# Performance work log

Hardware: AMD Instinct MI355X
Metric: run time of the kernel (lower is better)

Reference implementation:

```python
import jax, jax.numpy as jnp
import numpy as np

B, T, TA = 16, 512, 1024
D_REG, D_AUD, HID, HEADS = 512, 512, 256, 4
NREG = 4  # mouth, left_eye, right_eye, nose (dict order)
N = NREG * B * T + B * TA  # total graph nodes


def _build_edges():
    # Faithful, vectorized version of build_graph's edge construction (phoneme_times=None).
    bs = np.arange(B)[:, None]
    ts = np.arange(T)[None, :]
    src, dst = [], []
    # cross-region same-timestep edges, all ordered pairs i != j (edge_attr 0)
    for i in range(NREG):
        for j in range(NREG):
            if i != j:
                n1 = i * B * T + bs * T + ts
                n2 = j * B * T + bs * T + ts
                src.append(n1.ravel()); dst.append(n2.ravel())
    # temporal edges within each region (edge_attr 1)
    tt = np.arange(T - 1)[None, :]
    for i in range(NREG):
        n1 = i * B * T + bs * T + tt
        src.append(n1.ravel()); dst.append((n1 + 1).ravel())
    # eye (region idx 1,2) -> audio alignment edges (edge_attr 3)
    t_aud = (np.arange(T)[None, :] * TA) // T
    audio_start = NREG * B * T
    for i in (1, 2):
        n_eye = i * B * T + bs * T + ts
        n_aud = audio_start + bs * TA + t_aud
        src.append(n_eye.ravel()); dst.append(np.broadcast_to(n_aud, (B, T)).ravel())
    # self loops (PyG GATConv default add_self_loops=True)
    loops = np.arange(N)
    src.append(loops); dst.append(loops)
    return np.concatenate(src).astype(np.int32), np.concatenate(dst).astype(np.int32)


def setup_inputs() -> dict:
    key = jax.random.key(0)
    ks = iter(jax.random.split(key, 48))
    def rn(shape, scale=1.0):
        return jax.random.normal(next(ks), shape, dtype=jnp.float32) * jnp.float32(scale)
    src_np, dst_np = _build_edges()
    inp = {
        'mouth': rn((B, T, D_REG)), 'left_eye': rn((B, T, D_REG)),
        'right_eye': rn((B, T, D_REG)), 'nose': rn((B, T, D_REG)),
        'audio_embeddings': rn((B, TA, D_AUD)),
    }
    s = 1.0 / np.sqrt(D_REG)
    for name in ['mouth', 'left_eye', 'right_eye', 'nose']:
        inp['w_' + name] = rn((D_REG, HID), s)
        inp['b_' + name] = jnp.zeros((HID,), jnp.float32)
    inp['w_audio'] = rn((D_AUD, HID), 1.0 / np.sqrt(D_AUD))
    inp['b_audio'] = jnp.zeros((HID,), jnp.float32)
    # GAT layers: layer 0 in=HID, layers 1,2 in=HID*HEADS; layers 0,1 concat, layer 2 averages heads
    dims_in = [HID, HID * HEADS, HID * HEADS]
    for l, din in enumerate(dims_in):
        concat = l < 2
        inp[f'W{l}'] = rn((din, HEADS * HID), 1.0 / np.sqrt(din))
        inp[f'as{l}'] = rn((HEADS, HID), 0.1)
        inp[f'ad{l}'] = rn((HEADS, HID), 0.1)
        inp[f'bias{l}'] = jnp.zeros((HEADS * HID,) if concat else (HID,), jnp.float32)
    inp['ln_g'] = jnp.ones((HID,), jnp.float32)
    inp['ln_b'] = jnp.zeros((HID,), jnp.float32)
    inp['src'] = jnp.asarray(src_np)
    inp['dst'] = jnp.asarray(dst_np)
    return inp


def _gat(x, W, a_s, a_d, bias, src, dst, concat):
    # PyG GATConv (eval mode): gather -> per-head attention softmax over dst -> scatter-add
    H, C = a_s.shape
    h = (x @ W).reshape(-1, H, C)                      # [N,H,C]
    alpha_s = jnp.sum(h * a_s, -1)                     # [N,H]
    alpha_d = jnp.sum(h * a_d, -1)                     # [N,H]
    e = jax.nn.leaky_relu(alpha_s[src] + alpha_d[dst], 0.2)  # [E,H]
    m = jax.ops.segment_max(e, dst, num_segments=N)
    ex = jnp.exp(e - m[dst])
    denom = jax.ops.segment_sum(ex, dst, num_segments=N)
    alpha = ex / (denom[dst] + jnp.float32(1e-16))
    out = jax.ops.segment_sum(h[src] * alpha[:, :, None], dst, num_segments=N)  # [N,H,C]
    out = out.reshape(-1, H * C) if concat else out.mean(1)
    return out + bias


def _forward(mouth, left_eye, right_eye, nose, audio_embeddings,
             w_mouth, b_mouth, w_left_eye, b_left_eye, w_right_eye, b_right_eye,
             w_nose, b_nose, w_audio, b_audio,
             W0, as0, ad0, bias0, W1, as1, ad1, bias1, W2, as2, ad2, bias2,
             ln_g, ln_b, src, dst):
    x = jnp.concatenate([
        (mouth @ w_mouth + b_mouth).reshape(B * T, HID),
        (left_eye @ w_left_eye + b_left_eye).reshape(B * T, HID),
        (right_eye @ w_right_eye + b_right_eye).reshape(B * T, HID),
        (nose @ w_nose + b_nose).reshape(B * T, HID),
        (audio_embeddings @ w_audio + b_audio).reshape(B * TA, HID),
    ], axis=0)                                          # [N,HID]
    x = _gat(x, W0, as0, ad0, bias0, src, dst, True)    # [N,HID*HEADS]
    x = _gat(x, W1, as1, ad1, bias1, src, dst, True)    # [N,HID*HEADS]
    x = _gat(x, W2, as2, ad2, bias2, src, dst, False)   # [N,HID]
    mu = x.mean(-1, keepdims=True)
    var = jnp.mean(jnp.square(x - mu), -1, keepdims=True)
    x = (x - mu) / jnp.sqrt(var + jnp.float32(1e-5)) * ln_g + ln_b
    nodes_pb = NREG * T + TA
    return x.reshape(B, nodes_pb, HID).mean(1)          # [B,HID]


def reference(mouth, left_eye, right_eye, nose, audio_embeddings,
              w_mouth, b_mouth, w_left_eye, b_left_eye, w_right_eye, b_right_eye,
              w_nose, b_nose, w_audio, b_audio,
              W0, as0, ad0, bias0, W1, as1, ad1, bias1, W2, as2, ad2, bias2,
              ln_g, ln_b, src, dst):
    return _forward(mouth, left_eye, right_eye, nose, audio_embeddings,
                    w_mouth, b_mouth, w_left_eye, b_left_eye, w_right_eye, b_right_eye,
                    w_nose, b_nose, w_audio, b_audio,
                    W0, as0, ad0, bias0, W1, as1, ad1, bias1, W2, as2, ad2, bias2,
                    ln_g, ln_b, src, dst)
```

## Files before the change

### kernel.cpp

```cpp
#include <hip/hip_runtime.h>


typedef unsigned short u16;
typedef unsigned int u32;
typedef __bf16 bf16x8 __attribute__((ext_vector_type(8)));
typedef float f32x4 __attribute__((ext_vector_type(4)));

#define ASYNC16(gp, lp)                                                        \
  __builtin_amdgcn_global_load_lds(                                            \
      (const __attribute__((address_space(1))) void*)(gp),                     \
      (__attribute__((address_space(3))) void*)(lp), 16, 0, 0)

__device__ __forceinline__ u16 f2bf(float f) {
  union { float f; u32 u; } v; v.f = f;
  u32 u = v.u + 0x7FFFu + ((v.u >> 16) & 1u);
  return (u16)(u >> 16);
}
__device__ __forceinline__ float bf2f(u16 x) {
  union { u32 u; float f; } v; v.u = ((u32)x) << 16;
  return v.f;
}
__device__ __forceinline__ float4 cvt4(ushort4 s) {
  float4 r; r.x = bf2f(s.x); r.y = bf2f(s.y); r.z = bf2f(s.z); r.w = bf2f(s.w);
  return r;
}
__device__ __forceinline__ float lrelu(float v) { return v > 0.f ? v : 0.2f * v; }
__device__ __forceinline__ float dot4(float4 a, float4 b) {
  return a.x * b.x + a.y * b.y + a.z * b.z + a.w * b.w;
}
__device__ __forceinline__ float wred(float v) {
#pragma unroll
  for (int off = 32; off; off >>= 1) v += __shfl_down(v, off);
  return v;
}
__device__ __forceinline__ float wredx(float v) {
#pragma unroll
  for (int off = 32; off; off >>= 1) v += __shfl_xor(v, off);
  return v;
}

struct PK { const float* W[8]; u16* P[8]; int KB[8]; int NN[8]; int st[9]; };
__global__ __launch_bounds__(256) void pack_kernel(PK p) {
  const int f = blockIdx.x * 4 + (threadIdx.x >> 6);
  const int lane = threadIdx.x & 63;
  int e = 0;
  while (f >= p.st[e + 1]) ++e;
  const int local = f - p.st[e];
  const int KB = p.KB[e], N = p.NN[e];
  const int nt = local / KB, kb = local % KB;
  const float* W = p.W[e] + (size_t)(kb * 32 + (lane >> 4) * 8) * N + nt * 16 + (lane & 15);
  u16* dst = p.P[e] + ((size_t)local * 64 + lane) * 8;
  u16 o[8];
#pragma unroll
  for (int j = 0; j < 8; ++j) o[j] = f2bf(W[(size_t)j * N]);
  *(uint4*)dst = *(uint4*)o;
}

__global__ __launch_bounds__(256) void gemm_kernel(
    const u16* __restrict__ A, const u16* __restrict__ Bp, u16* __restrict__ C,
    int K, int ldc) {
  __shared__ __align__(16) u16 As[2][2][128 * 32];
  const int KB = K >> 5;
  const int KB2 = K >> 6;
  const int w = blockIdx.y * 8 + blockIdx.x;
  const int xcd = w & 7, m = w >> 3;
  const int blockCol = (m & 7) * 128;
  const int blockRow = ((m >> 3) * 8 + xcd) * 128;
  const int tid = threadIdx.x;
  const int wave = tid >> 6, lane = tid & 63;
  const int wr = (wave >> 1) * 64, wc = (wave & 1) * 64;
  const int lr = lane & 15, lq = lane >> 4;
  const int sRow = wave * 16 + (lane >> 2);
  const int sGc = (lane & 3) ^ ((sRow >> 1) & 3);
  const size_t aOff0 = (size_t)(blockRow + sRow) * K + sGc * 8;
  const size_t aOff1 = aOff0 + (size_t)64 * K;
  const int ldsOff0 = wave * 512;
  const int ldsOff1 = 2048 + wave * 512;

  const u16* Bn[4];
#pragma unroll
  for (int ni = 0; ni < 4; ++ni)
    Bn[ni] = Bp + ((size_t)(((blockCol + wc) >> 4) + ni) * KB) * 512 + lane * 8;

  f32x4 acc[4][4] = {};

#pragma unroll
  for (int h = 0; h < 2; ++h) {
    ASYNC16(A + aOff0 + h * 32, As[0][h] + ldsOff0);
    ASYNC16(A + aOff1 + h * 32, As[0][h] + ldsOff1);
  }
  __syncthreads();

  for (int kb2 = 0; kb2 < KB2; ++kb2) {
    const int cb = kb2 & 1;
    bf16x8 bfr[2][4];
#pragma unroll
    for (int h = 0; h < 2; ++h)
#pragma unroll
      for (int ni = 0; ni < 4; ++ni)
        bfr[h][ni] = *(const bf16x8*)(Bn[ni] + (size_t)(kb2 * 2 + h) * 512);
    if (kb2 + 1 < KB2) {
      const size_t k1 = (size_t)(kb2 + 1) * 64;
#pragma unroll
      for (int h = 0; h < 2; ++h) {
        ASYNC16(A + aOff0 + k1 + h * 32, As[cb ^ 1][h] + ldsOff0);
        ASYNC16(A + aOff1 + k1 + h * 32, As[cb ^ 1][h] + ldsOff1);
      }
    }
#pragma unroll
    for (int h = 0; h < 2; ++h) {
      const u16* cur = As[cb][h];
      bf16x8 af[4];
#pragma unroll
      for (int mi = 0; mi < 4; ++mi) {
        const int R = wr + mi * 16 + lr;
        const int cp = lq ^ ((R >> 1) & 3);
        af[mi] = *(const bf16x8*)(cur + R * 32 + cp * 8);
      }
#pragma unroll
      for (int mi = 0; mi < 4; ++mi)
#pragma unroll
        for (int ni = 0; ni < 4; ++ni)
          acc[mi][ni] = __builtin_amdgcn_mfma_f32_16x16x32_bf16(af[mi], bfr[h][ni],
                                                                acc[mi][ni], 0, 0, 0);
    }
    __syncthreads();
  }
#pragma unroll
  for (int mi = 0; mi < 4; ++mi)
#pragma unroll
    for (int ni = 0; ni < 4; ++ni) {
      const int col = blockCol + wc + ni * 16 + lr;
#pragma unroll
      for (int r = 0; r < 4; ++r) {
        const int row = blockRow + wr + mi * 16 + lq * 4 + r;
        C[(size_t)row * ldc + col] = f2bf(acc[mi][ni][r]);
      }
    }
}

struct ProjArgs { const float* x[5]; const u16* w[5]; const float* b[5]; };
__global__ __launch_bounds__(256) void proj_kernel(ProjArgs pa,
                                                   u16* __restrict__ C) {
  __shared__ __align__(16) u16 As[128 * 32];
  const int blockRow = blockIdx.y * 128, blockCol = blockIdx.x * 128;
  const int reg = blockRow >= 32768 ? 4 : (blockRow >> 13);
  const int regBase = reg == 4 ? 32768 : reg * 8192;
  const float* Af = pa.x[reg] + (size_t)(blockRow - regBase) * 512;
  const u16* Bp = pa.w[reg];
  const int tid = threadIdx.x;
  const int wave = tid >> 6, lane = tid & 63;
  const int wr = (wave >> 1) * 64, wc = (wave & 1) * 64;
  const int lr = lane & 15, lq = lane >> 4;
  const int rr = tid >> 2;
  const int cphys = tid & 3;
  const int sGc = cphys ^ ((tid >> 3) & 3);

  const u16* Bn[4];
#pragma unroll
  for (int ni = 0; ni < 4; ++ni)
    Bn[ni] = Bp + ((size_t)(((blockCol + wc) >> 4) + ni) * 16) * 512 + lane * 8;

  f32x4 acc[4][4] = {};

  for (int k0 = 0; k0 < 512; k0 += 32) {
    __syncthreads();
    bf16x8 bfr[4];
#pragma unroll
    for (int ni = 0; ni < 4; ++ni)
      bfr[ni] = *(const bf16x8*)(Bn[ni] + (size_t)k0 * 16);
#pragma unroll
    for (int i = 0; i < 2; ++i) {
      const int row = i * 64 + rr;
      const float* ap = Af + (size_t)row * 512 + k0 + sGc * 8;
      float4 f0 = *(const float4*)(ap);
      float4 f1 = *(const float4*)(ap + 4);
      uint4 pk;
      pk.x = (u32)f2bf(f0.x) | ((u32)f2bf(f0.y) << 16);
      pk.y = (u32)f2bf(f0.z) | ((u32)f2bf(f0.w) << 16);
      pk.z = (u32)f2bf(f1.x) | ((u32)f2bf(f1.y) << 16);
      pk.w = (u32)f2bf(f1.z) | ((u32)f2bf(f1.w) << 16);
      *(uint4*)(&As[row * 32 + cphys * 8]) = pk;
    }
    __syncthreads();
    bf16x8 af[4];
#pragma unroll
    for (int mi = 0; mi < 4; ++mi) {
      const int R = wr + mi * 16 + lr;
      const int cp = lq ^ ((R >> 1) & 3);
      af[mi] = *(const bf16x8*)(&As[R * 32 + cp * 8]);
    }
#pragma unroll
    for (int mi = 0; mi < 4; ++mi)
#pragma unroll
      for (int ni = 0; ni < 4; ++ni)
        acc[mi][ni] = __builtin_amdgcn_mfma_f32_16x16x32_bf16(af[mi], bfr[ni],
                                                              acc[mi][ni], 0, 0, 0);
  }
  const float* bias = pa.b[reg];
#pragma unroll
  for (int mi = 0; mi < 4; ++mi)
#pragma unroll
    for (int ni = 0; ni < 4; ++ni) {
      const int col = blockCol + wc + ni * 16 + lr;
      const float bv = bias[col];
#pragma unroll
      for (int r = 0; r < 4; ++r) {
        const int row = blockRow + wr + mi * 16 + lq * 4 + r;
        C[(size_t)row * 256 + col] = f2bf(acc[mi][ni][r] + bv);
      }
    }
}

template <bool MEAN>
__global__ __launch_bounds__(256) void agg_kernel(
    const u16* __restrict__ h, const float* __restrict__ a_s,
    const float* __restrict__ a_d, const float* __restrict__ bias,
    void* __restrict__ out) {
  extern __shared__ float red[];
  const int tid = threadIdx.x;
  const int head = tid >> 6, lane = tid & 63;
  const int c4 = tid * 4;
  const float4 sa = *(const float4*)(a_s + c4);
  const float4 da = *(const float4*)(a_d + c4);
  __shared__ float asL[4][4], adL[4][4], apL[4][4], aeS[4], aeD[4];
  __shared__ float alpha[4][4][5], alphaA[4][3];

  const int bt = blockIdx.x;
  const int b = bt >> 9, t = bt & 511;
  const bool hasPrev = t > 0;
  const int btp = hasPrev ? bt - 1 : bt;
  const int nodeE = 32768 + b * 1024 + 2 * t;
  const int nodeO = nodeE + 1;

  ushort4 rv[4], rp[4], raeR, raoR;
#pragma unroll
  for (int r = 0; r < 4; ++r)
    rv[r] = *(const ushort4*)(h + (size_t)(r * 8192 + bt) * 1024 + c4);
  raeR = *(const ushort4*)(h + (size_t)nodeE * 1024 + c4);
  raoR = *(const ushort4*)(h + (size_t)nodeO * 1024 + c4);
#pragma unroll
  for (int r = 0; r < 4; ++r)
    rp[r] = *(const ushort4*)(h + (size_t)(r * 8192 + btp) * 1024 + c4);

  float4 hv[4], hp[4];
#pragma unroll
  for (int r = 0; r < 4; ++r) hv[r] = cvt4(rv[r]);
  float4 hae = cvt4(raeR), hao = cvt4(raoR);
#pragma unroll
  for (int r = 0; r < 4; ++r) hp[r] = cvt4(rp[r]);

#pragma unroll
  for (int r = 0; r < 4; ++r) {
    float ss = wred(dot4(hv[r], sa));
    float dd = wred(dot4(hv[r], da));
    float sp = hasPrev ? wred(dot4(hp[r], sa)) : 0.f;
    if (lane == 0) { asL[r][head] = ss; adL[r][head] = dd; apL[r][head] = sp; }
  }
  {
    float se = wred(dot4(hae, sa));
    float de = wred(dot4(hae, da));
    if (lane == 0) { aeS[head] = se; aeD[head] = de; }
  }
  __syncthreads();
  if (tid < 16) {
    const int j = tid >> 2, hh = tid & 3;
    const float ad = adL[j][hh];
    float e[5];
#pragma unroll
    for (int r = 0; r < 4; ++r) e[r] = lrelu(asL[r][hh] + ad);
    int cnt = 4;
    if (hasPrev) { e[4] = lrelu(apL[j][hh] + ad); cnt = 5; }
    float mx = e[0];
    for (int k = 1; k < cnt; ++k) mx = fmaxf(mx, e[k]);
    float s = 0.f, ex[5];
    for (int k = 0; k < cnt; ++k) { ex[k] = __expf(e[k] - mx); s += ex[k]; }
    const float inv = 1.f / (s + 1e-16f);
#pragma unroll
    for (int k = 0; k < 5; ++k) alpha[j][hh][k] = (k < cnt) ? ex[k] * inv : 0.f;
  } else if (tid < 20) {
    const int hh = tid - 16;
    const float ad = aeD[hh];
    const float e0 = lrelu(aeS[hh] + ad);
    const float e1 = lrelu(asL[1][hh] + ad);
    const float e2 = lrelu(asL[2][hh] + ad);
    const float mx = fmaxf(e0, fmaxf(e1, e2));
    const float x0 = __expf(e0 - mx), x1 = __expf(e1 - mx), x2 = __expf(e2 - mx);
    const float inv = 1.f / (x0 + x1 + x2 + 1e-16f);
    alphaA[hh][0] = x0 * inv; alphaA[hh][1] = x1 * inv; alphaA[hh][2] = x2 * inv;
  }
  __syncthreads();

  float4 av[6];
#pragma unroll
  for (int j = 0; j < 4; ++j) {
    const float* al = &alpha[j][head][0];
    float4 acc;
    acc.x = al[0] * hv[0].x + al[1] * hv[1].x + al[2] * hv[2].x + al[3] * hv[3].x;
    acc.y = al[0] * hv[0].y + al[1] * hv[1].y + al[2] * hv[2].y + al[3] * hv[3].y;
    acc.z = al[0] * hv[0].z + al[1] * hv[1].z + al[2] * hv[2].z + al[3] * hv[3].z;
    acc.w = al[0] * hv[0].w + al[1] * hv[1].w + al[2] * hv[2].w + al[3] * hv[3].w;
    if (hasPrev) {
      const float a4 = al[4];
      acc.x += a4 * hp[j].x; acc.y += a4 * hp[j].y;
      acc.z += a4 * hp[j].z; acc.w += a4 * hp[j].w;
    }
    av[j] = acc;
  }
  {
    const float a0 = alphaA[head][0], a1 = alphaA[head][1], a2 = alphaA[head][2];
    float4 acc;
    acc.x = a0 * hae.x + a1 * hv[1].x + a2 * hv[2].x;
    acc.y = a0 * hae.y + a1 * hv[1].y + a2 * hv[2].y;
    acc.z = a0 * hae.z + a1 * hv[1].z + a2 * hv[2].z;
    acc.w = a0 * hae.w + a1 * hv[1].w + a2 * hv[2].w;
    av[4] = acc;
    av[5] = hao;
  }

  if constexpr (!MEAN) {
    const float4 bv = *(const float4*)(bias + c4);
    u16* ob = (u16*)out;
    size_t rows[6];
#pragma unroll
    for (int j = 0; j < 4; ++j) rows[j] = (size_t)(j * 8192 + bt);
    rows[4] = (size_t)nodeE; rows[5] = (size_t)nodeO;
#pragma unroll
    for (int k = 0; k < 6; ++k) {
      ushort4 o;
      o.x = f2bf(av[k].x + bv.x); o.y = f2bf(av[k].y + bv.y);
      o.z = f2bf(av[k].z + bv.z); o.w = f2bf(av[k].w + bv.w);
      *(ushort4*)(ob + rows[k] * 1024 + c4) = o;
    }
  } else {
#pragma unroll
    for (int k = 0; k < 6; ++k) *(float4*)(&red[k * 1024 + c4]) = av[k];
    __syncthreads();
    const float bb = bias[tid];
    float* of = (float*)out;
    size_t rows[6];
#pragma unroll
    for (int j = 0; j < 4; ++j) rows[j] = (size_t)(j * 8192 + bt);
    rows[4] = (size_t)nodeE; rows[5] = (size_t)nodeO;
#pragma unroll
    for (int k = 0; k < 6; ++k) {
      const float v = 0.25f * (red[k * 1024 + tid] + red[k * 1024 + tid + 256] +
                               red[k * 1024 + tid + 512] + red[k * 1024 + tid + 768]) + bb;
      of[rows[k] * 256 + tid] = v;
    }
  }
}

__global__ __launch_bounds__(256) void ln_pool_kernel(
    const float* __restrict__ xf, const float* __restrict__ g,
    const float* __restrict__ bb, float* __restrict__ part) {
  const int tid = threadIdx.x;
  const int wave = tid >> 6, lane = tid & 63;
  const int node0 = blockIdx.x * 64 + wave * 16;
  const float4 g4 = *(const float4*)(g + lane * 4);
  const float4 b4 = *(const float4*)(bb + lane * 4);
  float4 acc = {0.f, 0.f, 0.f, 0.f};
  for (int i = 0; i < 16; ++i) {
    const float4 v = *(const float4*)(xf + (size_t)(node0 + i) * 256 + lane * 4);
    const float s = wredx(v.x + v.y + v.z + v.w);
    const float q = wredx(v.x * v.x + v.y * v.y + v.z * v.z + v.w * v.w);
    const float mean = s * (1.f / 256.f);
    const float var = q * (1.f / 256.f) - mean * mean;
    const float rstd = rsqrtf(var + 1e-5f);
    acc.x += (v.x - mean) * rstd * g4.x + b4.x;
    acc.y += (v.y - mean) * rstd * g4.y + b4.y;
    acc.z += (v.z - mean) * rstd * g4.z + b4.z;
    acc.w += (v.w - mean) * rstd * g4.w + b4.w;
  }
  *(float4*)(part + (size_t)(blockIdx.x * 4 + wave) * 256 + lane * 4) = acc;
}

__global__ __launch_bounds__(256) void pool2_kernel(const float* __restrict__ part,
                                                    float* __restrict__ out) {
  const int chunk = blockIdx.x;
  const int c = threadIdx.x;
  float s = 0.f;
  for (int i = 0; i < 192; ++i) s += part[(size_t)(chunk * 192 + i) * 256 + c];
  out[chunk * 256 + c] = s * (1.f / 3072.f);
}

extern "C" void kernel_launch(void* const* d_in, const int* in_sizes, int n_in,
                              void* d_out, int out_size, void* d_ws, size_t ws_size,
                              hipStream_t stream) {
  const float* x_reg[4] = {(const float*)d_in[0], (const float*)d_in[1],
                           (const float*)d_in[2], (const float*)d_in[3]};
  const float* audio = (const float*)d_in[4];
  const float* w_reg[4] = {(const float*)d_in[5], (const float*)d_in[7],
                           (const float*)d_in[9], (const float*)d_in[11]};
  const float* b_reg[4] = {(const float*)d_in[6], (const float*)d_in[8],
                           (const float*)d_in[10], (const float*)d_in[12]};
  const float* w_aud = (const float*)d_in[13];
  const float* b_aud = (const float*)d_in[14];
  const float* Wl[3] = {(const float*)d_in[15], (const float*)d_in[19],
                        (const float*)d_in[23]};
  const float* as_in[3] = {(const float*)d_in[16], (const float*)d_in[20],
                           (const float*)d_in[24]};
  const float* ad_in[3] = {(const float*)d_in[17], (const float*)d_in[21],
                           (const float*)d_in[25]};
  const float* bias_l[3] = {(const float*)d_in[18], (const float*)d_in[22],
                            (const float*)d_in[26]};
  const float* ln_g = (const float*)d_in[27];
  const float* ln_b = (const float*)d_in[28];

  char* ws = (char*)d_ws;
  u16* h_bf = (u16*)ws;
  float* part = (float*)ws;
  u16* xb = (u16*)(ws + 100663296);
  float* xf = (float*)xb;
  u16* wt = (u16*)(ws + 201326592);

  u16* wtp[5];
  for (int r = 0; r < 5; ++r) wtp[r] = wt + (size_t)r * 131072;
  u16* wt0 = wt + 655360;
  u16* wt1 = wt + 917504;
  u16* wt2 = wt + 1966080;

  PK pk;
  for (int r = 0; r < 4; ++r) { pk.W[r] = w_reg[r]; pk.P[r] = wtp[r]; pk.KB[r] = 16; pk.NN[r] = 256; }
  pk.W[4] = w_aud; pk.P[4] = wtp[4]; pk.KB[4] = 16; pk.NN[4] = 256;
  pk.W[5] = Wl[0]; pk.P[5] = wt0; pk.KB[5] = 8;  pk.NN[5] = 1024;
  pk.W[6] = Wl[1]; pk.P[6] = wt1; pk.KB[6] = 32; pk.NN[6] = 1024;
  pk.W[7] = Wl[2]; pk.P[7] = wt2; pk.KB[7] = 32; pk.NN[7] = 1024;
  pk.st[0] = 0;
  {
    const int nfr[8] = {256, 256, 256, 256, 256, 512, 2048, 2048};
    int acc = 0;
    for (int e = 0; e < 8; ++e) { acc += nfr[e]; pk.st[e + 1] = acc; }
  }
  pack_kernel<<<pk.st[8] / 4, 256, 0, stream>>>(pk);

  ProjArgs pa;
  for (int r = 0; r < 4; ++r) { pa.x[r] = x_reg[r]; pa.w[r] = wtp[r]; pa.b[r] = b_reg[r]; }
  pa.x[4] = audio; pa.w[4] = wtp[4]; pa.b[4] = b_aud;
  proj_kernel<<<dim3(2, 384), 256, 0, stream>>>(pa, xb);

  const u16* wl[3] = {wt0, wt1, wt2};
  const int Kl[3] = {256, 1024, 1024};
  const size_t dynLds = 6 * 1024 * sizeof(float);
  for (int l = 0; l < 3; ++l) {
    gemm_kernel<<<dim3(8, 384), 256, 0, stream>>>(xb, wl[l], h_bf, Kl[l], 1024);
    if (l < 2)
      agg_kernel<false><<<8192, 256, 0, stream>>>(h_bf, as_in[l], ad_in[l],
                                                  bias_l[l], xb);
    else
      agg_kernel<true><<<8192, 256, dynLds, stream>>>(h_bf, as_in[l], ad_in[l],
                                                      bias_l[l], xf);
  }

  ln_pool_kernel<<<768, 256, 0, stream>>>(xf, ln_g, ln_b, part);
  pool2_kernel<<<16, 256, 0, stream>>>(part, (float*)d_out);
}
```

Measured before the change: 613.5 us.

## Rewrite GAT GEMM as 256x256 tile, 8-wave, 4-stage LDS pipeline

Replaces the 128x128-tile, 4-wave, double-buffered GEMM with a 256x256-tile kernel using 8 waves and a 4-deep ring of LDS buffers, where both A and B are now staged into LDS asynchronously. The K loop is split into two half-phases separated by barriers, with explicit vmcnt waits and s_setprio around the MFMA blocks so loads overlap compute. The aim is more reuse per tile and better hiding of global-memory latency. In exchange it uses 128 KB of LDS per block, limiting occupancy to one block per CU, and relies on hand-counted waitcnt values.

```diff
diff --git a/kernel.cpp b/kernel.cpp
--- a/kernel.cpp
+++ b/kernel.cpp
@@ -56,84 +56,115 @@
   *(uint4*)dst = *(uint4*)o;
 }
 
-__global__ __launch_bounds__(256) void gemm_kernel(
+__global__ __launch_bounds__(512, 1) void gemm_kernel(
     const u16* __restrict__ A, const u16* __restrict__ Bp, u16* __restrict__ C,
     int K, int ldc) {
-  __shared__ __align__(16) u16 As[2][2][128 * 32];
-  const int KB = K >> 5;
-  const int KB2 = K >> 6;
-  const int w = blockIdx.y * 8 + blockIdx.x;
-  const int xcd = w & 7, m = w >> 3;
-  const int blockCol = (m & 7) * 128;
-  const int blockRow = ((m >> 3) * 8 + xcd) * 128;
+  __shared__ __align__(16) u16 lds[4 * 16384];
+  const int NT = K >> 5;
+
+  const int orig = blockIdx.x;
+  const int x = orig & 7;
+  const int local = orig >> 3;
+  const int colTile = local & 3;
+  const int rowTile = x * 24 + (local >> 2);
+  const int blockRow = rowTile * 256;
+  const int blockCol = colTile * 256;
+
   const int tid = threadIdx.x;
   const int wave = tid >> 6, lane = tid & 63;
-  const int wr = (wave >> 1) * 64, wc = (wave & 1) * 64;
+  const int wm = wave >> 2, wn = wave & 3;
   const int lr = lane & 15, lq = lane >> 4;
-  const int sRow = wave * 16 + (lane >> 2);
-  const int sGc = (lane & 3) ^ ((sRow >> 1) & 3);
-  const size_t aOff0 = (size_t)(blockRow + sRow) * K + sGc * 8;
-  const size_t aOff1 = aOff0 + (size_t)64 * K;
-  const int ldsOff0 = wave * 512;
-  const int ldsOff1 = 2048 + wave * 512;
-
-  const u16* Bn[4];
-#pragma unroll
-  for (int ni = 0; ni < 4; ++ni)
-    Bn[ni] = Bp + ((size_t)(((blockCol + wc) >> 4) + ni) * KB) * 512 + lane * 8;
-
-  f32x4 acc[4][4] = {};
-
-#pragma unroll
-  for (int h = 0; h < 2; ++h) {
-    ASYNC16(A + aOff0 + h * 32, As[0][h] + ldsOff0);
-    ASYNC16(A + aOff1 + h * 32, As[0][h] + ldsOff1);
-  }
-  __syncthreads();
-
-  for (int kb2 = 0; kb2 < KB2; ++kb2) {
-    const int cb = kb2 & 1;
-    bf16x8 bfr[2][4];
-#pragma unroll
-    for (int h = 0; h < 2; ++h)
+  const int f0 = wave * 2, f1 = f0 + 1;
+
+  const int sR = lane >> 2;
+  const int sGc = (lane & 3) ^ ((lane >> 3) & 3);
+  const size_t aG0 = (size_t)(blockRow + f0 * 16 + sR) * K + sGc * 8;
+  const size_t aG1 = (size_t)(blockRow + f1 * 16 + sR) * K + sGc * 8;
+  const int ntBase = blockCol >> 4;
+  const size_t bG0 = (size_t)(ntBase + f0) * NT * 512 + lane * 8;
+  const size_t bG1 = (size_t)(ntBase + f1) * NT * 512 + lane * 8;
+
+  const int aFr = (wm * 128 + lr) * 32 + (lq ^ ((lr >> 1) & 3)) * 8;
+  const int bFr = wn * 2048 + lane * 8;
+
+#define STAGE_A(TS)                                                            \
+  do {                                                                         \
+    u16* db_ = &lds[((TS) & 3) * 16384];                                       \
+    ASYNC16(A + aG0 + (size_t)(TS) * 32, db_ + f0 * 512);                      \
+    ASYNC16(A + aG1 + (size_t)(TS) * 32, db_ + f1 * 512);                      \
+  } while (0)
+#define STAGE_B(TS)                                                            \
+  do {                                                                         \
+    u16* db_ = &lds[((TS) & 3) * 16384 + 8192];                                \
+    ASYNC16(Bp + bG0 + (size_t)(TS) * 512, db_ + f0 * 512);                    \
+    ASYNC16(Bp + bG1 + (size_t)(TS) * 512, db_ + f1 * 512);                    \
+  } while (0)
+
+  f32x4 acc[8][4] = {};
+
+  STAGE_A(0); STAGE_B(0);
+  STAGE_A(1); STAGE_B(1);
+  STAGE_A(2); STAGE_B(2);
+  asm volatile("s_waitcnt vmcnt(8)" ::: "memory");
+  asm volatile("s_barrier" ::: "memory");
+
+  for (int t = 0; t < NT; ++t) {
+    u16* Ab = &lds[(t & 3) * 16384];
+    u16* Bb = Ab + 8192;
+    const int ts = t + 3;
+    bf16x8 bfr[4], af[4];
+
+#pragma unroll
+    for (int ni = 0; ni < 4; ++ni)
+      bfr[ni] = *(const bf16x8*)(Bb + bFr + ni * 512);
+#pragma unroll
+    for (int i = 0; i < 4; ++i)
+      af[i] = *(const bf16x8*)(Ab + aFr + i * 512);
+    if (ts < NT) STAGE_A(ts);
+    asm volatile("s_barrier" ::: "memory");
+    __builtin_amdgcn_s_setprio(1);
+#pragma unroll
+    for (int i = 0; i < 4; ++i)
 #pragma unroll
       for (int ni = 0; ni < 4; ++ni)
-        bfr[h][ni] = *(const bf16x8*)(Bn[ni] + (size_t)(kb2 * 2 + h) * 512);
-    if (kb2 + 1 < KB2) {
-      const size_t k1 = (size_t)(kb2 + 1) * 64;
-#pragma unroll
-      for (int h = 0; h < 2; ++h) {
-        ASYNC16(A + aOff0 + k1 + h * 32, As[cb ^ 1][h] + ldsOff0);
-        ASYNC16(A + aOff1 + k1 + h * 32, As[cb ^ 1][h] + ldsOff1);
-      }
-    }
-#pragma unroll
-    for (int h = 0; h < 2; ++h) {
-      const u16* cur = As[cb][h];
-      bf16x8 af[4];
-#pragma unroll
-      for (int mi = 0; mi < 4; ++mi) {
-        const int R = wr + mi * 16 + lr;
-        const int cp = lq ^ ((R >> 1) & 3);
-        af[mi] = *(const bf16x8*)(cur + R * 32 + cp * 8);
-      }
-#pragma unroll
-      for (int mi = 0; mi < 4; ++mi)
-#pragma unroll
-        for (int ni = 0; ni < 4; ++ni)
-          acc[mi][ni] = __builtin_amdgcn_mfma_f32_16x16x32_bf16(af[mi], bfr[h][ni],
-                                                                acc[mi][ni], 0, 0, 0);
-    }
-    __syncthreads();
-  }
-#pragma unroll
-  for (int mi = 0; mi < 4; ++mi)
+        acc[i][ni] = __builtin_amdgcn_mfma_f32_16x16x32_bf16(af[i], bfr[ni],
+                                                             acc[i][ni], 0, 0, 0);
+    __builtin_amdgcn_s_setprio(0);
+    asm volatile("s_barrier" ::: "memory");
+
+#pragma unroll
+    for (int i = 0; i < 4; ++i)
+      af[i] = *(const bf16x8*)(Ab + aFr + (i + 4) * 512);
+    if (ts < NT) STAGE_B(ts);
+    if (t <= NT - 4) {
+      asm volatile("s_waitcnt vmcnt(8)" ::: "memory");
+    } else if (t == NT - 3) {
+      asm volatile("s_waitcnt vmcnt(4)" ::: "memory");
+    } else if (t == NT - 2) {
+      asm volatile("s_waitcnt vmcnt(0)" ::: "memory");
+    }
+    asm volatile("s_barrier" ::: "memory");
+    __builtin_amdgcn_s_setprio(1);
+#pragma unroll
+    for (int i = 0; i < 4; ++i)
+#pragma unroll
+      for (int ni = 0; ni < 4; ++ni)
+        acc[i + 4][ni] = __builtin_amdgcn_mfma_f32_16x16x32_bf16(af[i], bfr[ni],
+                                                                 acc[i + 4][ni], 0, 0, 0);
+    __builtin_amdgcn_s_setprio(0);
+    asm volatile("s_barrier" ::: "memory");
+  }
+#undef STAGE_A
+#undef STAGE_B
+
+#pragma unroll
+  for (int mi = 0; mi < 8; ++mi)
 #pragma unroll
     for (int ni = 0; ni < 4; ++ni) {
-      const int col = blockCol + wc + ni * 16 + lr;
+      const int col = blockCol + wn * 64 + ni * 16 + lr;
 #pragma unroll
       for (int r = 0; r < 4; ++r) {
-        const int row = blockRow + wr + mi * 16 + lq * 4 + r;
+        const int row = blockRow + wm * 128 + mi * 16 + lq * 4 + r;
         C[(size_t)row * ldc + col] = f2bf(acc[mi][ni][r]);
       }
     }
@@ -443,7 +474,7 @@
   const int Kl[3] = {256, 1024, 1024};
   const size_t dynLds = 6 * 1024 * sizeof(float);
   for (int l = 0; l < 3; ++l) {
-    gemm_kernel<<<dim3(8, 384), 256, 0, stream>>>(xb, wl[l], h_bf, Kl[l], 1024);
+    gemm_kernel<<<768, 512, 0, stream>>>(xb, wl[l], h_bf, Kl[l], 1024);
     if (l < 2)
       agg_kernel<false><<<8192, 256, 0, stream>>>(h_bf, as_in[l], ad_in[l],
                                                   bias_l[l], xb);
```

Result: no change. 618.6 us (+0.8%).

## Deepen GEMM A-tile prefetch to a 4-buffer pipeline with explicit vmcnt waits

Applied to the files above, without the earlier changes.

Replaces the double-buffered 64-wide K step in the GEMM with a four-slot ring of 32-wide A tiles in LDS, prefetching three stages ahead. It uses hand-written s_waitcnt vmcnt counts and raw s_barrier in place of __syncthreads. The aim is to hide more global-load latency and to lighten each barrier. The risk is that the hard-coded vmcnt counts must match the number of outstanding loads, B-fragment loads included, or the kernel could read LDS before the data lands.

```diff
diff --git a/kernel.cpp b/kernel.cpp
--- a/kernel.cpp
+++ b/kernel.cpp
@@ -59,9 +59,8 @@
 __global__ __launch_bounds__(256) void gemm_kernel(
     const u16* __restrict__ A, const u16* __restrict__ Bp, u16* __restrict__ C,
     int K, int ldc) {
-  __shared__ __align__(16) u16 As[2][2][128 * 32];
-  const int KB = K >> 5;
-  const int KB2 = K >> 6;
+  __shared__ __align__(16) u16 As[4][128 * 32];
+  const int NT = K >> 5;
   const int w = blockIdx.y * 8 + blockIdx.x;
   const int xcd = w & 7, m = w >> 3;
   const int blockCol = (m & 7) * 128;
@@ -80,52 +79,52 @@
   const u16* Bn[4];
 #pragma unroll
   for (int ni = 0; ni < 4; ++ni)
-    Bn[ni] = Bp + ((size_t)(((blockCol + wc) >> 4) + ni) * KB) * 512 + lane * 8;
+    Bn[ni] = Bp + ((size_t)(((blockCol + wc) >> 4) + ni) * NT) * 512 + lane * 8;
 
   f32x4 acc[4][4] = {};
 
-#pragma unroll
-  for (int h = 0; h < 2; ++h) {
-    ASYNC16(A + aOff0 + h * 32, As[0][h] + ldsOff0);
-    ASYNC16(A + aOff1 + h * 32, As[0][h] + ldsOff1);
-  }
-  __syncthreads();
-
-  for (int kb2 = 0; kb2 < KB2; ++kb2) {
-    const int cb = kb2 & 1;
-    bf16x8 bfr[2][4];
-#pragma unroll
-    for (int h = 0; h < 2; ++h)
+#define STAGE(TS)                                                              \
+  do {                                                                         \
+    u16* db_ = As[(TS) & 3];                                                   \
+    ASYNC16(A + aOff0 + (size_t)(TS) * 32, db_ + ldsOff0);                     \
+    ASYNC16(A + aOff1 + (size_t)(TS) * 32, db_ + ldsOff1);                     \
+  } while (0)
+
+  STAGE(0); STAGE(1); STAGE(2);
+  asm volatile("s_waitcnt vmcnt(4)" ::: "memory");
+  asm volatile("s_barrier" ::: "memory");
+
+  for (int t = 0; t < NT; ++t) {
+    bf16x8 bfr[4];
+#pragma unroll
+    for (int ni = 0; ni < 4; ++ni)
+      bfr[ni] = *(const bf16x8*)(Bn[ni] + (size_t)t * 512);
+    const u16* cur = As[t & 3];
+    bf16x8 af[4];
+#pragma unroll
+    for (int mi = 0; mi < 4; ++mi) {
+      const int R = wr + mi * 16 + lr;
+      const int cp = lq ^ ((R >> 1) & 3);
+      af[mi] = *(const bf16x8*)(cur + R * 32 + cp * 8);
+    }
+    if (t + 3 < NT) STAGE(t + 3);
+#pragma unroll
+    for (int mi = 0; mi < 4; ++mi)
 #pragma unroll
       for (int ni = 0; ni < 4; ++ni)
-        bfr[h][ni] = *(const bf16x8*)(Bn[ni] + (size_t)(kb2 * 2 + h) * 512);
-    if (kb2 + 1 < KB2) {
-      const size_t k1 = (size_t)(kb2 + 1) * 64;
-#pragma unroll
-      for (int h = 0; h < 2; ++h) {
-        ASYNC16(A + aOff0 + k1 + h * 32, As[cb ^ 1][h] + ldsOff0);
-        ASYNC16(A + aOff1 + k1 + h * 32, As[cb ^ 1][h] + ldsOff1);
-      }
-    }
-#pragma unroll
-    for (int h = 0; h < 2; ++h) {
-      const u16* cur = As[cb][h];
-      bf16x8 af[4];
-#pragma unroll
-      for (int mi = 0; mi < 4; ++mi) {
-        const int R = wr + mi * 16 + lr;
-        const int cp = lq ^ ((R >> 1) & 3);
-        af[mi] = *(const bf16x8*)(cur + R * 32 + cp * 8);
-      }
-#pragma unroll
-      for (int mi = 0; mi < 4; ++mi)
-#pragma unroll
-        for (int ni = 0; ni < 4; ++ni)
-          acc[mi][ni] = __builtin_amdgcn_mfma_f32_16x16x32_bf16(af[mi], bfr[h][ni],
-                                                                acc[mi][ni], 0, 0, 0);
-    }
-    __syncthreads();
-  }
+        acc[mi][ni] = __builtin_amdgcn_mfma_f32_16x16x32_bf16(af[mi], bfr[ni],
+                                                              acc[mi][ni], 0, 0, 0);
+    if (t <= NT - 4) {
+      asm volatile("s_waitcnt vmcnt(12)" ::: "memory");
+    } else if (t == NT - 3) {
+      asm volatile("s_waitcnt vmcnt(10)" ::: "memory");
+    } else if (t == NT - 2) {
+      asm volatile("s_waitcnt vmcnt(8)" ::: "memory");
+    }
+    asm volatile("s_barrier" ::: "memory");
+  }
+#undef STAGE
+
 #pragma unroll
   for (int mi = 0; mi < 4; ++mi)
 #pragma unroll
```

Result: slower. 700.4 us (+14.2%).

## Switch GAT GEMM to 32x32x16 MFMA with repacked weights; remap agg block order

Applied to the files above, without the earlier changes.

The layer GEMM now uses 32x32x16 bf16 MFMA tiles (2x2 per wave) in place of 16x16x32 (4x4 per wave), and the weight pack kernel is changed to emit fragments in the matching 32-column layout. The goal is fewer MFMA issues and fewer LDS A-fragment reads per FLOP. The aggregation kernel also permutes block indices so that neighbouring blocks are spread across XCDs, aiming at better L2 locality. The epilogue store pattern changes, and the larger accumulator tile raises register pressure.

```diff
diff --git a/kernel.cpp b/kernel.cpp
--- a/kernel.cpp
+++ b/kernel.cpp
@@ -5,6 +5,7 @@
 typedef unsigned int u32;
 typedef __bf16 bf16x8 __attribute__((ext_vector_type(8)));
 typedef float f32x4 __attribute__((ext_vector_type(4)));
+typedef float f32x16 __attribute__((ext_vector_type(16)));
 
 #define ASYNC16(gp, lp)                                                        \
   __builtin_amdgcn_global_load_lds(                                            \
@@ -48,7 +49,11 @@
   const int local = f - p.st[e];
   const int KB = p.KB[e], N = p.NN[e];
   const int nt = local / KB, kb = local % KB;
-  const float* W = p.W[e] + (size_t)(kb * 32 + (lane >> 4) * 8) * N + nt * 16 + (lane & 15);
+  const float* W;
+  if (e < 5)
+    W = p.W[e] + (size_t)(kb * 32 + (lane >> 4) * 8) * N + nt * 16 + (lane & 15);
+  else
+    W = p.W[e] + (size_t)(kb * 16 + (lane >> 5) * 8) * N + nt * 32 + (lane & 31);
   u16* dst = p.P[e] + ((size_t)local * 64 + lane) * 8;
   u16 o[8];
 #pragma unroll
@@ -60,8 +65,8 @@
     const u16* __restrict__ A, const u16* __restrict__ Bp, u16* __restrict__ C,
     int K, int ldc) {
   __shared__ __align__(16) u16 As[2][2][128 * 32];
-  const int KB = K >> 5;
   const int KB2 = K >> 6;
+  const int NT16 = K >> 4;
   const int w = blockIdx.y * 8 + blockIdx.x;
   const int xcd = w & 7, m = w >> 3;
   const int blockCol = (m & 7) * 128;
@@ -69,7 +74,7 @@
   const int tid = threadIdx.x;
   const int wave = tid >> 6, lane = tid & 63;
   const int wr = (wave >> 1) * 64, wc = (wave & 1) * 64;
-  const int lr = lane & 15, lq = lane >> 4;
+  const int lc = lane & 31, kq = lane >> 5;
   const int sRow = wave * 16 + (lane >> 2);
   const int sGc = (lane & 3) ^ ((sRow >> 1) & 3);
   const size_t aOff0 = (size_t)(blockRow + sRow) * K + sGc * 8;
@@ -77,12 +82,12 @@
   const int ldsOff0 = wave * 512;
   const int ldsOff1 = 2048 + wave * 512;
 
-  const u16* Bn[4];
-#pragma unroll
-  for (int ni = 0; ni < 4; ++ni)
-    Bn[ni] = Bp + ((size_t)(((blockCol + wc) >> 4) + ni) * KB) * 512 + lane * 8;
-
-  f32x4 acc[4][4] = {};
+  const u16* Bn[2];
+#pragma unroll
+  for (int ni = 0; ni < 2; ++ni)
+    Bn[ni] = Bp + ((size_t)(((blockCol + wc) >> 5) + ni) * NT16) * 512 + lane * 8;
+
+  f32x16 acc[2][2] = {};
 
 #pragma unroll
   for (int h = 0; h < 2; ++h) {
@@ -95,10 +100,10 @@
     const int cb = kb2 & 1;
     bf16x8 bfr[2][4];
 #pragma unroll
-    for (int h = 0; h < 2; ++h)
-#pragma unroll
-      for (int ni = 0; ni < 4; ++ni)
-        bfr[h][ni] = *(const bf16x8*)(Bn[ni] + (size_t)(kb2 * 2 + h) * 512);
+    for (int ni = 0; ni < 2; ++ni)
+#pragma unroll
+      for (int c = 0; c < 4; ++c)
+        bfr[ni][c] = *(const bf16x8*)(Bn[ni] + (size_t)(kb2 * 4 + c) * 512);
     if (kb2 + 1 < KB2) {
       const size_t k1 = (size_t)(kb2 + 1) * 64;
 #pragma unroll
@@ -110,30 +115,36 @@
 #pragma unroll
     for (int h = 0; h < 2; ++h) {
       const u16* cur = As[cb][h];
-      bf16x8 af[4];
-#pragma unroll
-      for (int mi = 0; mi < 4; ++mi) {
-        const int R = wr + mi * 16 + lr;
-        const int cp = lq ^ ((R >> 1) & 3);
-        af[mi] = *(const bf16x8*)(cur + R * 32 + cp * 8);
+      bf16x8 af[2][2];
+#pragma unroll
+      for (int mi = 0; mi < 2; ++mi) {
+        const int R = wr + mi * 32 + lc;
+        const int swz = (R >> 1) & 3;
+#pragma unroll
+        for (int kk = 0; kk < 2; ++kk) {
+          const int cp = (kk * 2 + kq) ^ swz;
+          af[mi][kk] = *(const bf16x8*)(cur + R * 32 + cp * 8);
+        }
       }
 #pragma unroll
-      for (int mi = 0; mi < 4; ++mi)
-#pragma unroll
-        for (int ni = 0; ni < 4; ++ni)
-          acc[mi][ni] = __builtin_amdgcn_mfma_f32_16x16x32_bf16(af[mi], bfr[h][ni],
-                                                                acc[mi][ni], 0, 0, 0);
+      for (int kk = 0; kk < 2; ++kk)
+#pragma unroll
+        for (int mi = 0; mi < 2; ++mi)
+#pragma unroll
+          for (int ni = 0; ni < 2; ++ni)
+            acc[mi][ni] = __builtin_amdgcn_mfma_f32_32x32x16_bf16(
+                af[mi][kk], bfr[ni][h * 2 + kk], acc[mi][ni], 0, 0, 0);
     }
     __syncthreads();
   }
 #pragma unroll
-  for (int mi = 0; mi < 4; ++mi)
-#pragma unroll
-    for (int ni = 0; ni < 4; ++ni) {
-      const int col = blockCol + wc + ni * 16 + lr;
-#pragma unroll
-      for (int r = 0; r < 4; ++r) {
-        const int row = blockRow + wr + mi * 16 + lq * 4 + r;
+  for (int mi = 0; mi < 2; ++mi)
+#pragma unroll
+    for (int ni = 0; ni < 2; ++ni) {
+      const int col = blockCol + wc + ni * 32 + lc;
+#pragma unroll
+      for (int r = 0; r < 16; ++r) {
+        const int row = blockRow + wr + mi * 32 + (r & 3) + 8 * (r >> 2) + 4 * kq;
         C[(size_t)row * ldc + col] = f2bf(acc[mi][ni][r]);
       }
     }
@@ -226,7 +237,8 @@
   __shared__ float asL[4][4], adL[4][4], apL[4][4], aeS[4], aeD[4];
   __shared__ float alpha[4][4][5], alphaA[4][3];
 
-  const int bt = blockIdx.x;
+  const int bid = blockIdx.x;
+  const int bt = ((bid & 7) << 10) | (bid >> 3);
   const int b = bt >> 9, t = bt & 511;
   const bool hasPrev = t > 0;
   const int btp = hasPrev ? bt - 1 : bt;
@@ -423,9 +435,9 @@
   PK pk;
   for (int r = 0; r < 4; ++r) { pk.W[r] = w_reg[r]; pk.P[r] = wtp[r]; pk.KB[r] = 16; pk.NN[r] = 256; }
   pk.W[4] = w_aud; pk.P[4] = wtp[4]; pk.KB[4] = 16; pk.NN[4] = 256;
-  pk.W[5] = Wl[0]; pk.P[5] = wt0; pk.KB[5] = 8;  pk.NN[5] = 1024;
-  pk.W[6] = Wl[1]; pk.P[6] = wt1; pk.KB[6] = 32; pk.NN[6] = 1024;
-  pk.W[7] = Wl[2]; pk.P[7] = wt2; pk.KB[7] = 32; pk.NN[7] = 1024;
+  pk.W[5] = Wl[0]; pk.P[5] = wt0; pk.KB[5] = 16; pk.NN[5] = 1024;
+  pk.W[6] = Wl[1]; pk.P[6] = wt1; pk.KB[6] = 64; pk.NN[6] = 1024;
+  pk.W[7] = Wl[2]; pk.P[7] = wt2; pk.KB[7] = 64; pk.NN[7] = 1024;
   pk.st[0] = 0;
   {
     const int nfr[8] = {256, 256, 256, 256, 256, 512, 2048, 2048};
```

After: 636.5 us. +3.8%, slower.
